# Kernel optimization log

Hardware: AMD Instinct MI355X
Metric: run time of the kernel (lower is better)

The kernel has to match this reference:

```python
import jax, jax.numpy as jnp
import numpy as np

N_CELLS = 50000
DEG = 32
NNZ = N_CELLS * DEG
D_IN = 64
D_OUT = 64
NEG_SLOPE = 0.2


def setup_inputs() -> dict:
    key = jax.random.key(0)
    k0, k1, k2, k3, k4 = jax.random.split(key, 5)
    x_source = jax.random.normal(k0, (N_CELLS, D_IN), jnp.float32)
    # COO indices of the sparse neighborhood matrix N: DEG entries per row
    edge_rows = jnp.repeat(jnp.arange(N_CELLS, dtype=jnp.int32), DEG)
    edge_cols = jax.random.randint(k1, (NNZ,), 0, N_CELLS, dtype=jnp.int32)
    neighborhood_values = jax.random.uniform(k2, (NNZ,), jnp.float32)
    # xavier_uniform-ish scales (exact init irrelevant for correctness baseline)
    W0 = jax.random.normal(k3, (D_IN, D_OUT), jnp.float32) * (1.414 / np.sqrt(D_IN))
    a0 = jax.random.normal(k4, (2 * D_OUT, 1), jnp.float32) * 0.1
    return {
        "x_source": x_source,
        "edge_rows": edge_rows,
        "edge_cols": edge_cols,
        "neighborhood_values": neighborhood_values,
        "W0": W0,
        "a0": a0,
    }


def reference(x_source, edge_rows, edge_cols, neighborhood_values, W0, a0):
    # message = X W_p  : [n_cells, d_out]
    message = x_source @ W0
    d = message.shape[1]
    # [X_i || X_j] a  ==  (X_i a_src) + (X_j a_dst); compute node-level dot first,
    # then gather per edge (avoids materializing [nnz, 2d] concat)
    a_src = a0[:d, 0]
    a_dst = a0[d:, 0]
    node_src = message @ a_src  # [n_cells]
    node_dst = message @ a_dst  # [n_cells]
    e = jax.nn.leaky_relu(node_src[edge_rows] + node_dst[edge_cols],
                          negative_slope=NEG_SLOPE)  # [nnz]
    # sparse_row_norm: divide each edge value by its row sum (softmax=False path)
    row_sum = jax.ops.segment_sum(e, edge_rows, num_segments=N_CELLS)
    att = e / row_sum[edge_rows]
    # Hadamard product N^1 \odot A_1, then SpMM with message
    vals = neighborhood_values * att  # [nnz]
    out = jax.ops.segment_sum(vals[:, None] * message[edge_cols], edge_rows,
                              num_segments=N_CELLS)  # [n_cells, d_out]
    # update_func='relu'
    return jax.nn.relu(out)
```

## Files before the change

### kernel.cpp

```cpp
#include <hip/hip_runtime.h>
#include <hip/hip_fp16.h>

#define N_CELLS 50000
#define DEG 32
#define DIM 64
#define NEG_SLOPE 0.2
#define NPAIRS (N_CELLS / 2)

__global__ __launch_bounds__(256)
void gat_nodes(const float* __restrict__ x,
               const float* __restrict__ W0,
               const float* __restrict__ a0,
               double* __restrict__ ns,
               double* __restrict__ nd) {
  __shared__ double2 p_s[DIM];

  const int tid = threadIdx.x;
  if (tid < DIM) {
    double ps = 0.0, pd = 0.0;
    const float4* w4 = (const float4*)(W0 + tid * DIM);
#pragma unroll
    for (int q = 0; q < DIM / 4; ++q) {
      float4 w = w4[q];
      ps = fma((double)w.x, (double)a0[4 * q + 0], ps);
      ps = fma((double)w.y, (double)a0[4 * q + 1], ps);
      ps = fma((double)w.z, (double)a0[4 * q + 2], ps);
      ps = fma((double)w.w, (double)a0[4 * q + 3], ps);
      pd = fma((double)w.x, (double)a0[DIM + 4 * q + 0], pd);
      pd = fma((double)w.y, (double)a0[DIM + 4 * q + 1], pd);
      pd = fma((double)w.z, (double)a0[DIM + 4 * q + 2], pd);
      pd = fma((double)w.w, (double)a0[DIM + 4 * q + 3], pd);
    }
    p_s[tid] = make_double2(ps, pd);
  }
  __syncthreads();

  const int r = blockIdx.x * 256 + tid;
  if (r >= N_CELLS) return;

  const float4* x4 = (const float4*)(x + (size_t)r * DIM);
  double s0 = 0.0, s1 = 0.0, d0 = 0.0, d1 = 0.0;
#pragma unroll
  for (int q = 0; q < DIM / 4; ++q) {
    float4 v = x4[q];
    double2 p0 = p_s[4 * q + 0], p1 = p_s[4 * q + 1];
    double2 p2 = p_s[4 * q + 2], p3 = p_s[4 * q + 3];
    s0 = fma((double)v.x, p0.x, s0); d0 = fma((double)v.x, p0.y, d0);
    s1 = fma((double)v.y, p1.x, s1); d1 = fma((double)v.y, p1.y, d1);
    s0 = fma((double)v.z, p2.x, s0); d0 = fma((double)v.z, p2.y, d0);
    s1 = fma((double)v.w, p3.x, s1); d1 = fma((double)v.w, p3.y, d1);
  }
  ns[r] = s0 + s1;
  nd[r] = d0 + d1;
}

__global__ __launch_bounds__(256, 4)
void gat_msg(const float* __restrict__ x,
             const float* __restrict__ W0,
             __half* __restrict__ m2) {
  const int lane = threadIdx.x & 63;

  float w0c[DIM];
#pragma unroll
  for (int k = 0; k < DIM; ++k) w0c[k] = W0[k * DIM + lane];

  const int gwave = blockIdx.x * 4 + (threadIdx.x >> 6);
  const int nwaves = gridDim.x * 4;

  for (int r = gwave; r < N_CELLS; r += nwaves) {
    const float xv = x[(size_t)r * DIM + lane];
    const int xi = __float_as_int(xv);
    float m0 = 0.f, m1 = 0.f, m2a = 0.f, m3 = 0.f;
#pragma unroll
    for (int k = 0; k < DIM; k += 4) {
      m0 = fmaf(__int_as_float(__builtin_amdgcn_readlane(xi, k + 0)), w0c[k + 0], m0);
      m1 = fmaf(__int_as_float(__builtin_amdgcn_readlane(xi, k + 1)), w0c[k + 1], m1);
      m2a = fmaf(__int_as_float(__builtin_amdgcn_readlane(xi, k + 2)), w0c[k + 2], m2a);
      m3 = fmaf(__int_as_float(__builtin_amdgcn_readlane(xi, k + 3)), w0c[k + 3], m3);
    }
    const float m = (m0 + m1) + (m2a + m3);
    m2[(size_t)r * DIM + lane] = __float2half(m);
  }
}

__global__ __launch_bounds__(256, 4)
void gat_edges(const __half* __restrict__ m2,
               const int* __restrict__ ecol,
               const float* __restrict__ nv,
               const double* __restrict__ ns,
               const double* __restrict__ nd,
               float* __restrict__ out) {
  __shared__ __align__(16) float w_s[4][2][DEG];
  __shared__ __align__(16) int c_s[4][2][DEG];

  const int lane = threadIdx.x & 63;
  const int wid = threadIdx.x >> 6;
  const int half = lane >> 5;
  const int sub = lane & 31;

  const int gwave = blockIdx.x * 4 + wid;
  const int nwaves = gridDim.x * 4;
  const unsigned* xp = (const unsigned*)m2;

  int col_c = 0; float nv_c = 0.0f; double nd_c = 0.0, ns_c = 0.0;
  if (gwave < NPAIRS) {
    const int eidx = 2 * gwave * DEG + lane;
    col_c = __builtin_nontemporal_load(ecol + eidx);
    nv_c = __builtin_nontemporal_load(nv + eidx);
    nd_c = nd[col_c];
    ns_c = ns[2 * gwave + half];
  }

  for (int p = gwave; p < NPAIRS; p += nwaves) {
    const int r0 = 2 * p;
    const float nvv = nv_c;
    const double ndv = nd_c;
    const double nsv = ns_c;

    double z = nsv + ndv;
    double e = (z >= 0.0) ? z : NEG_SLOPE * z;
    double rs = e;
#pragma unroll
    for (int m = 16; m >= 1; m >>= 1) rs += __shfl_xor(rs, m, 64);
    w_s[wid][half][sub] = nvv * ((float)e / (float)rs);
    c_s[wid][half][sub] = col_c;

    const int pn = p + nwaves;
    const int psafe = (pn < NPAIRS) ? pn : p;
    const int eidxn = 2 * psafe * DEG + lane;
    col_c = __builtin_nontemporal_load(ecol + eidxn);
    nv_c = __builtin_nontemporal_load(nv + eidxn);
    ns_c = ns[2 * psafe + half];

    const int* cs = c_s[wid][half];
    const float* wsp = w_s[wid][half];
    float ax = 0.0f, ay = 0.0f;
#pragma unroll
    for (int b = 0; b < DEG; b += 16) {
      const int4 ca = ((const int4*)(cs + b))[0];
      const int4 cb = ((const int4*)(cs + b))[1];
      const int4 cc = ((const int4*)(cs + b))[2];
      const int4 cd = ((const int4*)(cs + b))[3];
      const float4 wa = ((const float4*)(wsp + b))[0];
      const float4 wb = ((const float4*)(wsp + b))[1];
      const float4 wc = ((const float4*)(wsp + b))[2];
      const float4 wd = ((const float4*)(wsp + b))[3];
      unsigned pk[16];
      pk[0]  = xp[(size_t)ca.x * (DIM / 2) + sub];
      pk[1]  = xp[(size_t)ca.y * (DIM / 2) + sub];
      pk[2]  = xp[(size_t)ca.z * (DIM / 2) + sub];
      pk[3]  = xp[(size_t)ca.w * (DIM / 2) + sub];
      pk[4]  = xp[(size_t)cb.x * (DIM / 2) + sub];
      pk[5]  = xp[(size_t)cb.y * (DIM / 2) + sub];
      pk[6]  = xp[(size_t)cb.z * (DIM / 2) + sub];
      pk[7]  = xp[(size_t)cb.w * (DIM / 2) + sub];
      pk[8]  = xp[(size_t)cc.x * (DIM / 2) + sub];
      pk[9]  = xp[(size_t)cc.y * (DIM / 2) + sub];
      pk[10] = xp[(size_t)cc.z * (DIM / 2) + sub];
      pk[11] = xp[(size_t)cc.w * (DIM / 2) + sub];
      pk[12] = xp[(size_t)cd.x * (DIM / 2) + sub];
      pk[13] = xp[(size_t)cd.y * (DIM / 2) + sub];
      pk[14] = xp[(size_t)cd.z * (DIM / 2) + sub];
      pk[15] = xp[(size_t)cd.w * (DIM / 2) + sub];
      float ax0 = 0.f, ay0 = 0.f, ax1 = 0.f, ay1 = 0.f;
      const float wj[16] = {wa.x, wa.y, wa.z, wa.w, wb.x, wb.y, wb.z, wb.w,
                            wc.x, wc.y, wc.z, wc.w, wd.x, wd.y, wd.z, wd.w};
#pragma unroll
      for (int i = 0; i < 16; i += 2) {
        float2 v0 = __half22float2(*(const __half2*)&pk[i]);
        float2 v1 = __half22float2(*(const __half2*)&pk[i + 1]);
        ax0 = fmaf(wj[i], v0.x, ax0);
        ay0 = fmaf(wj[i], v0.y, ay0);
        ax1 = fmaf(wj[i + 1], v1.x, ax1);
        ay1 = fmaf(wj[i + 1], v1.y, ay1);
      }
      ax += ax0 + ax1;
      ay += ay0 + ay1;
    }

    nd_c = nd[col_c];

    const size_t o = (size_t)(r0 + half) * DIM + 2 * sub;
    __builtin_nontemporal_store(fmaxf(ax, 0.0f), out + o);
    __builtin_nontemporal_store(fmaxf(ay, 0.0f), out + o + 1);
  }
}

extern "C" void kernel_launch(void* const* d_in, const int* in_sizes, int n_in,
                              void* d_out, int out_size, void* d_ws, size_t ws_size,
                              hipStream_t stream) {
  const float* x = (const float*)d_in[0];
  const int* ecol = (const int*)d_in[2];
  const float* nv = (const float*)d_in[3];
  const float* W0 = (const float*)d_in[4];
  const float* a0 = (const float*)d_in[5];
  float* out = (float*)d_out;

  __half* m2 = (__half*)d_ws;
  double* ns = (double*)((char*)d_ws + (size_t)N_CELLS * DIM * sizeof(__half));
  double* nd = ns + N_CELLS;

  hipLaunchKernelGGL(gat_nodes, dim3((N_CELLS + 255) / 256), dim3(256), 0, stream,
                     x, W0, a0, ns, nd);
  hipLaunchKernelGGL(gat_msg, dim3(800), dim3(256), 0, stream, x, W0, m2);
  hipLaunchKernelGGL(gat_edges, dim3(1280), dim3(256), 0, stream,
                     m2, ecol, nv, ns, nd, out);
}
```

Measured before the change: 128.9 us.

## Fuse node-score and message kernels; issue all 32 gathers before attention math

```diff
diff --git a/kernel.cpp b/kernel.cpp
--- a/kernel.cpp
+++ b/kernel.cpp
@@ -8,14 +8,17 @@
 #define NPAIRS (N_CELLS / 2)
 
 __global__ __launch_bounds__(256)
-void gat_nodes(const float* __restrict__ x,
-               const float* __restrict__ W0,
-               const float* __restrict__ a0,
-               double* __restrict__ ns,
-               double* __restrict__ nd) {
+void gat_prep(const float* __restrict__ x,
+              const float* __restrict__ W0,
+              const float* __restrict__ a0,
+              __half* __restrict__ m2,
+              double* __restrict__ ns,
+              double* __restrict__ nd) {
   __shared__ double2 p_s[DIM];
 
   const int tid = threadIdx.x;
+  const int lane = tid & 63;
+
   if (tid < DIM) {
     double ps = 0.0, pd = 0.0;
     const float4* w4 = (const float4*)(W0 + tid * DIM);
@@ -33,53 +36,48 @@
     }
     p_s[tid] = make_double2(ps, pd);
   }
+
+  {
+    float w0c[DIM];
+#pragma unroll
+    for (int k = 0; k < DIM; ++k) w0c[k] = W0[k * DIM + lane];
+
+    const int gwave = blockIdx.x * 4 + (tid >> 6);
+    const int nwaves = gridDim.x * 4;
+    for (int r = gwave; r < N_CELLS; r += nwaves) {
+      const float xv = x[(size_t)r * DIM + lane];
+      const int xi = __float_as_int(xv);
+      float m0 = 0.f, m1 = 0.f, m2a = 0.f, m3 = 0.f;
+#pragma unroll
+      for (int k = 0; k < DIM; k += 4) {
+        m0 = fmaf(__int_as_float(__builtin_amdgcn_readlane(xi, k + 0)), w0c[k + 0], m0);
+        m1 = fmaf(__int_as_float(__builtin_amdgcn_readlane(xi, k + 1)), w0c[k + 1], m1);
+        m2a = fmaf(__int_as_float(__builtin_amdgcn_readlane(xi, k + 2)), w0c[k + 2], m2a);
+        m3 = fmaf(__int_as_float(__builtin_amdgcn_readlane(xi, k + 3)), w0c[k + 3], m3);
+      }
+      m2[(size_t)r * DIM + lane] = __float2half((m0 + m1) + (m2a + m3));
+    }
+  }
+
   __syncthreads();
 
-  const int r = blockIdx.x * 256 + tid;
-  if (r >= N_CELLS) return;
-
-  const float4* x4 = (const float4*)(x + (size_t)r * DIM);
-  double s0 = 0.0, s1 = 0.0, d0 = 0.0, d1 = 0.0;
-#pragma unroll
-  for (int q = 0; q < DIM / 4; ++q) {
-    float4 v = x4[q];
-    double2 p0 = p_s[4 * q + 0], p1 = p_s[4 * q + 1];
-    double2 p2 = p_s[4 * q + 2], p3 = p_s[4 * q + 3];
-    s0 = fma((double)v.x, p0.x, s0); d0 = fma((double)v.x, p0.y, d0);
-    s1 = fma((double)v.y, p1.x, s1); d1 = fma((double)v.y, p1.y, d1);
-    s0 = fma((double)v.z, p2.x, s0); d0 = fma((double)v.z, p2.y, d0);
-    s1 = fma((double)v.w, p3.x, s1); d1 = fma((double)v.w, p3.y, d1);
-  }
-  ns[r] = s0 + s1;
-  nd[r] = d0 + d1;
-}
-
-__global__ __launch_bounds__(256, 4)
-void gat_msg(const float* __restrict__ x,
-             const float* __restrict__ W0,
-             __half* __restrict__ m2) {
-  const int lane = threadIdx.x & 63;
-
-  float w0c[DIM];
-#pragma unroll
-  for (int k = 0; k < DIM; ++k) w0c[k] = W0[k * DIM + lane];
-
-  const int gwave = blockIdx.x * 4 + (threadIdx.x >> 6);
-  const int nwaves = gridDim.x * 4;
-
-  for (int r = gwave; r < N_CELLS; r += nwaves) {
-    const float xv = x[(size_t)r * DIM + lane];
-    const int xi = __float_as_int(xv);
-    float m0 = 0.f, m1 = 0.f, m2a = 0.f, m3 = 0.f;
-#pragma unroll
-    for (int k = 0; k < DIM; k += 4) {
-      m0 = fmaf(__int_as_float(__builtin_amdgcn_readlane(xi, k + 0)), w0c[k + 0], m0);
-      m1 = fmaf(__int_as_float(__builtin_amdgcn_readlane(xi, k + 1)), w0c[k + 1], m1);
-      m2a = fmaf(__int_as_float(__builtin_amdgcn_readlane(xi, k + 2)), w0c[k + 2], m2a);
-      m3 = fmaf(__int_as_float(__builtin_amdgcn_readlane(xi, k + 3)), w0c[k + 3], m3);
-    }
-    const float m = (m0 + m1) + (m2a + m3);
-    m2[(size_t)r * DIM + lane] = __float2half(m);
+  const int gtid = blockIdx.x * 256 + tid;
+  const int nthreads = gridDim.x * 256;
+  for (int r = gtid; r < N_CELLS; r += nthreads) {
+    const float4* x4 = (const float4*)(x + (size_t)r * DIM);
+    double s0 = 0.0, s1 = 0.0, d0 = 0.0, d1 = 0.0;
+#pragma unroll
+    for (int q = 0; q < DIM / 4; ++q) {
+      float4 v = x4[q];
+      double2 p0 = p_s[4 * q + 0], p1 = p_s[4 * q + 1];
+      double2 p2 = p_s[4 * q + 2], p3 = p_s[4 * q + 3];
+      s0 = fma((double)v.x, p0.x, s0); d0 = fma((double)v.x, p0.y, d0);
+      s1 = fma((double)v.y, p1.x, s1); d1 = fma((double)v.y, p1.y, d1);
+      s0 = fma((double)v.z, p2.x, s0); d0 = fma((double)v.z, p2.y, d0);
+      s1 = fma((double)v.w, p3.x, s1); d1 = fma((double)v.w, p3.y, d1);
+    }
+    ns[r] = s0 + s1;
+    nd[r] = d0 + d1;
   }
 }
 
@@ -117,13 +115,56 @@
     const double ndv = nd_c;
     const double nsv = ns_c;
 
+    c_s[wid][half][sub] = col_c;
+    const int* cs = c_s[wid][half];
+    const int4 c0 = ((const int4*)cs)[0];
+    const int4 c1 = ((const int4*)cs)[1];
+    const int4 c2 = ((const int4*)cs)[2];
+    const int4 c3 = ((const int4*)cs)[3];
+    const int4 c4 = ((const int4*)cs)[4];
+    const int4 c5 = ((const int4*)cs)[5];
+    const int4 c6 = ((const int4*)cs)[6];
+    const int4 c7 = ((const int4*)cs)[7];
+    unsigned pk[32];
+    pk[0]  = xp[(size_t)c0.x * (DIM / 2) + sub];
+    pk[1]  = xp[(size_t)c0.y * (DIM / 2) + sub];
+    pk[2]  = xp[(size_t)c0.z * (DIM / 2) + sub];
+    pk[3]  = xp[(size_t)c0.w * (DIM / 2) + sub];
+    pk[4]  = xp[(size_t)c1.x * (DIM / 2) + sub];
+    pk[5]  = xp[(size_t)c1.y * (DIM / 2) + sub];
+    pk[6]  = xp[(size_t)c1.z * (DIM / 2) + sub];
+    pk[7]  = xp[(size_t)c1.w * (DIM / 2) + sub];
+    pk[8]  = xp[(size_t)c2.x * (DIM / 2) + sub];
+    pk[9]  = xp[(size_t)c2.y * (DIM / 2) + sub];
+    pk[10] = xp[(size_t)c2.z * (DIM / 2) + sub];
+    pk[11] = xp[(size_t)c2.w * (DIM / 2) + sub];
+    pk[12] = xp[(size_t)c3.x * (DIM / 2) + sub];
+    pk[13] = xp[(size_t)c3.y * (DIM / 2) + sub];
+    pk[14] = xp[(size_t)c3.z * (DIM / 2) + sub];
+    pk[15] = xp[(size_t)c3.w * (DIM / 2) + sub];
+    pk[16] = xp[(size_t)c4.x * (DIM / 2) + sub];
+    pk[17] = xp[(size_t)c4.y * (DIM / 2) + sub];
+    pk[18] = xp[(size_t)c4.z * (DIM / 2) + sub];
+    pk[19] = xp[(size_t)c4.w * (DIM / 2) + sub];
+    pk[20] = xp[(size_t)c5.x * (DIM / 2) + sub];
+    pk[21] = xp[(size_t)c5.y * (DIM / 2) + sub];
+    pk[22] = xp[(size_t)c5.z * (DIM / 2) + sub];
+    pk[23] = xp[(size_t)c5.w * (DIM / 2) + sub];
+    pk[24] = xp[(size_t)c6.x * (DIM / 2) + sub];
+    pk[25] = xp[(size_t)c6.y * (DIM / 2) + sub];
+    pk[26] = xp[(size_t)c6.z * (DIM / 2) + sub];
+    pk[27] = xp[(size_t)c6.w * (DIM / 2) + sub];
+    pk[28] = xp[(size_t)c7.x * (DIM / 2) + sub];
+    pk[29] = xp[(size_t)c7.y * (DIM / 2) + sub];
+    pk[30] = xp[(size_t)c7.z * (DIM / 2) + sub];
+    pk[31] = xp[(size_t)c7.w * (DIM / 2) + sub];
+
     double z = nsv + ndv;
     double e = (z >= 0.0) ? z : NEG_SLOPE * z;
     double rs = e;
 #pragma unroll
     for (int m = 16; m >= 1; m >>= 1) rs += __shfl_xor(rs, m, 64);
     w_s[wid][half][sub] = nvv * ((float)e / (float)rs);
-    c_s[wid][half][sub] = col_c;
 
     const int pn = p + nwaves;
     const int psafe = (pn < NPAIRS) ? pn : p;
@@ -132,43 +173,21 @@
     nv_c = __builtin_nontemporal_load(nv + eidxn);
     ns_c = ns[2 * psafe + half];
 
-    const int* cs = c_s[wid][half];
     const float* wsp = w_s[wid][half];
     float ax = 0.0f, ay = 0.0f;
 #pragma unroll
-    for (int b = 0; b < DEG; b += 16) {
-      const int4 ca = ((const int4*)(cs + b))[0];
-      const int4 cb = ((const int4*)(cs + b))[1];
-      const int4 cc = ((const int4*)(cs + b))[2];
-      const int4 cd = ((const int4*)(cs + b))[3];
-      const float4 wa = ((const float4*)(wsp + b))[0];
-      const float4 wb = ((const float4*)(wsp + b))[1];
-      const float4 wc = ((const float4*)(wsp + b))[2];
-      const float4 wd = ((const float4*)(wsp + b))[3];
-      unsigned pk[16];
-      pk[0]  = xp[(size_t)ca.x * (DIM / 2) + sub];
-      pk[1]  = xp[(size_t)ca.y * (DIM / 2) + sub];
-      pk[2]  = xp[(size_t)ca.z * (DIM / 2) + sub];
-      pk[3]  = xp[(size_t)ca.w * (DIM / 2) + sub];
-      pk[4]  = xp[(size_t)cb.x * (DIM / 2) + sub];
-      pk[5]  = xp[(size_t)cb.y * (DIM / 2) + sub];
-      pk[6]  = xp[(size_t)cb.z * (DIM / 2) + sub];
-      pk[7]  = xp[(size_t)cb.w * (DIM / 2) + sub];
-      pk[8]  = xp[(size_t)cc.x * (DIM / 2) + sub];
-      pk[9]  = xp[(size_t)cc.y * (DIM / 2) + sub];
-      pk[10] = xp[(size_t)cc.z * (DIM / 2) + sub];
-      pk[11] = xp[(size_t)cc.w * (DIM / 2) + sub];
-      pk[12] = xp[(size_t)cd.x * (DIM / 2) + sub];
-      pk[13] = xp[(size_t)cd.y * (DIM / 2) + sub];
-      pk[14] = xp[(size_t)cd.z * (DIM / 2) + sub];
-      pk[15] = xp[(size_t)cd.w * (DIM / 2) + sub];
-      float ax0 = 0.f, ay0 = 0.f, ax1 = 0.f, ay1 = 0.f;
+    for (int g = 0; g < 2; ++g) {
+      const float4 wa = ((const float4*)wsp)[4 * g + 0];
+      const float4 wb = ((const float4*)wsp)[4 * g + 1];
+      const float4 wc = ((const float4*)wsp)[4 * g + 2];
+      const float4 wd = ((const float4*)wsp)[4 * g + 3];
       const float wj[16] = {wa.x, wa.y, wa.z, wa.w, wb.x, wb.y, wb.z, wb.w,
                             wc.x, wc.y, wc.z, wc.w, wd.x, wd.y, wd.z, wd.w};
+      float ax0 = 0.f, ay0 = 0.f, ax1 = 0.f, ay1 = 0.f;
 #pragma unroll
       for (int i = 0; i < 16; i += 2) {
-        float2 v0 = __half22float2(*(const __half2*)&pk[i]);
-        float2 v1 = __half22float2(*(const __half2*)&pk[i + 1]);
+        float2 v0 = __half22float2(*(const __half2*)&pk[16 * g + i]);
+        float2 v1 = __half22float2(*(const __half2*)&pk[16 * g + i + 1]);
         ax0 = fmaf(wj[i], v0.x, ax0);
         ay0 = fmaf(wj[i], v0.y, ay0);
         ax1 = fmaf(wj[i + 1], v1.x, ax1);
@@ -180,9 +199,10 @@
 
     nd_c = nd[col_c];
 
-    const size_t o = (size_t)(r0 + half) * DIM + 2 * sub;
-    __builtin_nontemporal_store(fmaxf(ax, 0.0f), out + o);
-    __builtin_nontemporal_store(fmaxf(ay, 0.0f), out + o + 1);
+    union { float f[2]; double d; } o;
+    o.f[0] = fmaxf(ax, 0.0f);
+    o.f[1] = fmaxf(ay, 0.0f);
+    __builtin_nontemporal_store(o.d, (double*)(out + (size_t)(r0 + half) * DIM) + sub);
   }
 }
 
@@ -200,9 +220,8 @@
   double* ns = (double*)((char*)d_ws + (size_t)N_CELLS * DIM * sizeof(__half));
   double* nd = ns + N_CELLS;
 
-  hipLaunchKernelGGL(gat_nodes, dim3((N_CELLS + 255) / 256), dim3(256), 0, stream,
-                     x, W0, a0, ns, nd);
-  hipLaunchKernelGGL(gat_msg, dim3(800), dim3(256), 0, stream, x, W0, m2);
+  hipLaunchKernelGGL(gat_prep, dim3(800), dim3(256), 0, stream,
+                     x, W0, a0, m2, ns, nd);
   hipLaunchKernelGGL(gat_edges, dim3(1280), dim3(256), 0, stream,
                      m2, ecol, nv, ns, nd, out);
 }
```

After: 150.7 us. 16.9% more time.
